# Kernel optimization log

Measured on AMD Instinct MI355X. Metric: run time of the kernel, lower is better.

The kernel has to match this reference:

```python
import jax, jax.numpy as jnp
import numpy as np


def _bilinear_align_corners(img, H, W):
    """Bilinear resize of img [B,K,h,w] to [B,K,H,W], align_corners=True."""
    h, w = img.shape[-2], img.shape[-1]
    ys = jnp.linspace(0.0, h - 1.0, H)
    xs = jnp.linspace(0.0, w - 1.0, W)
    y0 = jnp.clip(jnp.floor(ys).astype(jnp.int32), 0, h - 1)
    y1 = jnp.minimum(y0 + 1, h - 1)
    x0 = jnp.clip(jnp.floor(xs).astype(jnp.int32), 0, w - 1)
    x1 = jnp.minimum(x0 + 1, w - 1)
    wy = (ys - y0.astype(img.dtype))[:, None]   # [H,1]
    wx = (xs - x0.astype(img.dtype))            # [W]
    r0 = img[:, :, y0, :]                        # [B,K,H,w]
    r1 = img[:, :, y1, :]
    top = r0[..., x0] * (1.0 - wx) + r0[..., x1] * wx   # [B,K,H,W]
    bot = r1[..., x0] * (1.0 - wx) + r1[..., x1] * wx
    return top * (1.0 - wy) + bot * wy


def setup_inputs() -> dict:
    key = jax.random.key(0)
    k1, k2, k3 = jax.random.split(key, 3)
    B, C, h, w = 8, 256, 64, 64
    H, W = 512, 512
    K = 21
    feature_map = jax.random.normal(k1, (B, C, h, w), dtype=jnp.float32)
    x = jax.random.uniform(k2, (B, 3, H, W), dtype=jnp.float32)
    W_cls = jax.random.normal(k3, (K, C), dtype=jnp.float32) * 0.02
    b_cls = jnp.zeros((K,), dtype=jnp.float32)
    return {"feature_map": feature_map, "x": x, "W_cls": W_cls, "b_cls": b_cls}


def reference(feature_map, x, W_cls, b_cls):
    # 1x1 conv == channel contraction
    logits = jnp.einsum('bchw,kc->bkhw', feature_map, W_cls) + b_cls[None, :, None, None]
    seg = jax.nn.softmax(logits, axis=1)                      # [B,K,h,w]
    H, W = x.shape[2], x.shape[3]
    seg = _bilinear_align_corners(seg, H, W)                  # [B,K,H,W]
    xi = jnp.transpose(x, (0, 2, 3, 1))                       # [B,H,W,3]
    # q[b,k,c] = mean over (H,W) of x * seg_k  (the per-class loop, fused)
    q = jnp.einsum('bhwc,bkhw->bkc', xi, seg) / (H * W)       # [B,K,3]
    # attn[b,k,h,w] = sum_c x[b,h,w,c] * q[b,k,c]
    segments_by_color = jnp.einsum('bhwc,bkc->bkhw', xi, q)   # [B,K,H,W]
    return segments_by_color
```

## Files before the change

### kernel.cpp

```cpp
#include <hip/hip_runtime.h>
#include <math.h>

#define NB 8
#define NC 256
#define HS 64
#define WSM 64
#define HL 512
#define WL 512
#define NK 21
#define PS (HS*WSM)
#define PL (HL*WL)

#define WT_ELEMS (NK*NC)
#define WT_BLOCKS ((WT_ELEMS+63)/64)

typedef float fx4 __attribute__((ext_vector_type(4)));


__global__ __launch_bounds__(64) void k_prep(
    const float* __restrict__ Wc, float* __restrict__ Wt, float* __restrict__ q)
{
    int blk = blockIdx.x;
    int tid = threadIdx.x;
    if (blk < WT_BLOCKS) {
        int i = blk * 64 + tid;
        if (i < WT_ELEMS) {
            int c = i / NK;
            int k = i - c*NK;
            Wt[c*32 + k] = Wc[k*NC + c];
        }
    } else {
        for (int i = tid; i < NB*NK*3; i += 64) q[i] = 0.f;
    }
}

__global__ __launch_bounds__(256) void k_fused(
    const float* __restrict__ fm, const float* __restrict__ Wt,
    const float* __restrict__ bc, const float* __restrict__ x,
    float* __restrict__ q)
{
    int id = blockIdx.x;
    int swz = (id & 7) * 64 + (id >> 3);
    int b = swz >> 6;
    int h = swz & 63;
    int lane = threadIdx.x & 63;
    int wv   = threadIdx.x >> 6;
    int p = h * 64 + lane;

    __shared__ float tmp[3][WL];
    __shared__ float sA[3][64];
    __shared__ float red[4][NK][64];

    const float scale = 63.0f / 511.0f;
    const float inv_scale = 511.0f / 63.0f;

    if (wv < 3) {
        int Ylo = max(0,    (int)floorf((h - 1) * inv_scale) - 1);
        int Yhi = min(HL-1, (int)ceilf ((h + 1) * inv_scale) + 1);
        const float* xc = x + (size_t)(b*3 + wv) * PL;
        fx4 acc0 = {0.f,0.f,0.f,0.f}, acc1 = {0.f,0.f,0.f,0.f};
        for (int Y = Ylo; Y <= Yhi; ++Y) {
            float fs = Y * scale;
            int i0 = (int)fs; if (i0 > HS-1) i0 = HS-1;
            float f = fs - (float)i0;
            int i1 = min(i0 + 1, HS-1);
            float wt = (i0 == h ? 1.f - f : 0.f) + (i1 == h ? f : 0.f);
            const fx4* xr = (const fx4*)(xc + (size_t)Y * WL);
            acc0 += wt * xr[lane];
            acc1 += wt * xr[lane + 64];
        }
        fx4* t4 = (fx4*)tmp[wv];
        t4[lane]      = acc0;
        t4[lane + 64] = acc1;
        const int w_ = lane;
        int Xlo = max(0,    (int)floorf((w_ - 1) * inv_scale) - 1);
        int Xhi = min(WL-1, (int)ceilf ((w_ + 1) * inv_scale) + 1);
        float a = 0.f;
        for (int X = Xlo; X <= Xhi; ++X) {
            float fs = X * scale;
            int i0 = (int)fs; if (i0 > WSM-1) i0 = WSM-1;
            float f = fs - (float)i0;
            int i1 = min(i0 + 1, WSM-1);
            float wt = (i0 == w_ ? 1.f - f : 0.f) + (i1 == w_ ? f : 0.f);
            a = fmaf(wt, tmp[wv][X], a);
        }
        sA[wv][lane] = a;
    }

    float part[NK];
    #pragma unroll
    for (int k = 0; k < NK; ++k) part[k] = 0.f;

    const float* fmb = fm + (size_t)b * NC * PS + (size_t)(wv * 64) * PS + p;
    #pragma unroll 8
    for (int cc = 0; cc < 64; ++cc) {
        float v = __builtin_nontemporal_load(fmb + (size_t)cc * PS);
        const float* w = Wt + (wv * 64 + cc) * 32;
        #pragma unroll
        for (int k = 0; k < NK; ++k) part[k] = fmaf(v, w[k], part[k]);
    }

    #pragma unroll
    for (int k = 0; k < NK; ++k) red[wv][k][lane] = part[k];
    __syncthreads();

    float logit[NK];
    #pragma unroll
    for (int k = 0; k < NK; ++k)
        logit[k] = bc[k] + ((red[0][k][lane] + red[1][k][lane])
                          + (red[2][k][lane] + red[3][k][lane]));

    float m = logit[0];
    #pragma unroll
    for (int k = 1; k < NK; ++k) m = fmaxf(m, logit[k]);
    float s = 0.f;
    #pragma unroll
    for (int k = 0; k < NK; ++k) { logit[k] = __expf(logit[k] - m); s += logit[k]; }
    float inv = 1.f / s;

    float a0 = sA[0][lane], a1 = sA[1][lane], a2 = sA[2][lane];

    float* qb = q + b * NK * 3;
    for (int k = wv; k < NK; k += 4) {
        float sv = logit[k] * inv;
        float r0 = sv * a0, r1 = sv * a1, r2 = sv * a2;
        #pragma unroll
        for (int off = 32; off; off >>= 1) {
            r0 += __shfl_down(r0, off);
            r1 += __shfl_down(r1, off);
            r2 += __shfl_down(r2, off);
        }
        if (lane == 0) {
            atomicAdd(qb + k*3 + 0, r0);
            atomicAdd(qb + k*3 + 1, r1);
            atomicAdd(qb + k*3 + 2, r2);
        }
    }
}

__global__ __launch_bounds__(256) void k_out(
    const float* __restrict__ x, const float* __restrict__ q,
    float* __restrict__ out)
{
    __shared__ float sq[NK*3];
    int tid = threadIdx.x;
    int b = blockIdx.y;
    if (tid < NK*3) sq[tid] = q[b*NK*3 + tid] * (1.0f / (float)PL);
    __syncthreads();

    int p4 = blockIdx.x * 256 + tid;
    const fx4* xb = (const fx4*)(x + (size_t)b * 3 * PL);
    fx4 x0 = xb[p4];
    fx4 x1 = xb[PL/4 + p4];
    fx4 x2 = xb[2*(PL/4) + p4];
    fx4* ob = (fx4*)(out + (size_t)b * NK * PL);
    #pragma unroll
    for (int k = 0; k < NK; ++k) {
        fx4 o = sq[k*3+0]*x0 + sq[k*3+1]*x1 + sq[k*3+2]*x2;
        __builtin_nontemporal_store(o, ob + (size_t)k * (PL/4) + p4);
    }
}

extern "C" void kernel_launch(void* const* d_in, const int* in_sizes, int n_in,
                              void* d_out, int out_size, void* d_ws, size_t ws_size,
                              hipStream_t stream)
{
    const float* fm = (const float*)d_in[0];
    const float* x  = (const float*)d_in[1];
    const float* Wc = (const float*)d_in[2];
    const float* bc = (const float*)d_in[3];
    float* out = (float*)d_out;

    float* ws = (float*)d_ws;
    float* Wt = ws;
    float* q  = Wt + 8192;

    k_prep<<<WT_BLOCKS + 1, 64, 0, stream>>>(Wc, Wt, q);
    k_fused<<<NB*HS, 256, 0, stream>>>(fm, Wt, bc, x, q);
    k_out<<<dim3(PL/4/256, NB), 256, 0, stream>>>(x, q, out);
}
```

Baseline: 268.8 us.

## Drop prep kernel: stage weights in LDS and replace atomics with partial sums

Removes the separate weight-transpose and zero-init kernel. Each fused block now loads and transposes the classifier weights into shared memory, using a stride of 22, before its channel contraction. Per-row results go to a partials buffer instead of being added atomically. The output kernel then reduces the 64 partials per batch in shared memory before broadcasting q. This saves one launch and the atomic contention, but every block reloads the weights, uses more LDS (which may lower occupancy), and each output block repeats the partial-sum reduction.

```diff
diff --git a/kernel.cpp b/kernel.cpp
--- a/kernel.cpp
+++ b/kernel.cpp
@@ -12,32 +12,14 @@
 #define PL (HL*WL)
 
 #define WT_ELEMS (NK*NC)
-#define WT_BLOCKS ((WT_ELEMS+63)/64)
 
 typedef float fx4 __attribute__((ext_vector_type(4)));
 
 
-__global__ __launch_bounds__(64) void k_prep(
-    const float* __restrict__ Wc, float* __restrict__ Wt, float* __restrict__ q)
-{
-    int blk = blockIdx.x;
-    int tid = threadIdx.x;
-    if (blk < WT_BLOCKS) {
-        int i = blk * 64 + tid;
-        if (i < WT_ELEMS) {
-            int c = i / NK;
-            int k = i - c*NK;
-            Wt[c*32 + k] = Wc[k*NC + c];
-        }
-    } else {
-        for (int i = tid; i < NB*NK*3; i += 64) q[i] = 0.f;
-    }
-}
-
 __global__ __launch_bounds__(256) void k_fused(
-    const float* __restrict__ fm, const float* __restrict__ Wt,
+    const float* __restrict__ fm, const float* __restrict__ Wc,
     const float* __restrict__ bc, const float* __restrict__ x,
-    float* __restrict__ q)
+    float* __restrict__ qpart)
 {
     int id = blockIdx.x;
     int swz = (id & 7) * 64 + (id >> 3);
@@ -47,9 +29,16 @@
     int wv   = threadIdx.x >> 6;
     int p = h * 64 + lane;
 
+    __shared__ float sWt[NC*22];
     __shared__ float tmp[3][WL];
     __shared__ float sA[3][64];
     __shared__ float red[4][NK][64];
+
+    for (int i = threadIdx.x; i < WT_ELEMS; i += 256) {
+        int k = i >> 8;
+        int c = i & 255;
+        sWt[c*22 + k] = Wc[i];
+    }
 
     const float scale = 63.0f / 511.0f;
     const float inv_scale = 511.0f / 63.0f;
@@ -87,6 +76,8 @@
         sA[wv][lane] = a;
     }
 
+    __syncthreads();
+
     float part[NK];
     #pragma unroll
     for (int k = 0; k < NK; ++k) part[k] = 0.f;
@@ -95,7 +86,7 @@
     #pragma unroll 8
     for (int cc = 0; cc < 64; ++cc) {
         float v = __builtin_nontemporal_load(fmb + (size_t)cc * PS);
-        const float* w = Wt + (wv * 64 + cc) * 32;
+        const float* w = sWt + (wv * 64 + cc) * 22;
         #pragma unroll
         for (int k = 0; k < NK; ++k) part[k] = fmaf(v, w[k], part[k]);
     }
@@ -120,7 +111,7 @@
 
     float a0 = sA[0][lane], a1 = sA[1][lane], a2 = sA[2][lane];
 
-    float* qb = q + b * NK * 3;
+    float* qb = qpart + (size_t)(b*64 + h) * 64;
     for (int k = wv; k < NK; k += 4) {
         float sv = logit[k] * inv;
         float r0 = sv * a0, r1 = sv * a1, r2 = sv * a2;
@@ -131,21 +122,32 @@
             r2 += __shfl_down(r2, off);
         }
         if (lane == 0) {
-            atomicAdd(qb + k*3 + 0, r0);
-            atomicAdd(qb + k*3 + 1, r1);
-            atomicAdd(qb + k*3 + 2, r2);
+            qb[k*3 + 0] = r0;
+            qb[k*3 + 1] = r1;
+            qb[k*3 + 2] = r2;
         }
     }
 }
 
 __global__ __launch_bounds__(256) void k_out(
-    const float* __restrict__ x, const float* __restrict__ q,
+    const float* __restrict__ x, const float* __restrict__ qpart,
     float* __restrict__ out)
 {
+    __shared__ float lq[64*64];
     __shared__ float sq[NK*3];
     int tid = threadIdx.x;
     int b = blockIdx.y;
-    if (tid < NK*3) sq[tid] = q[b*NK*3 + tid] * (1.0f / (float)PL);
+
+    const fx4* qp4 = (const fx4*)(qpart + (size_t)b * 64 * 64);
+    fx4* lq4 = (fx4*)lq;
+    #pragma unroll
+    for (int j = 0; j < 4; ++j) lq4[tid + j*256] = qp4[tid + j*256];
+    __syncthreads();
+    if (tid < NK*3) {
+        float s = 0.f;
+        for (int j = 0; j < 64; ++j) s += lq[j*64 + tid];
+        sq[tid] = s * (1.0f / (float)PL);
+    }
     __syncthreads();
 
     int p4 = blockIdx.x * 256 + tid;
@@ -171,11 +173,8 @@
     const float* bc = (const float*)d_in[3];
     float* out = (float*)d_out;
 
-    float* ws = (float*)d_ws;
-    float* Wt = ws;
-    float* q  = Wt + 8192;
+    float* qpart = (float*)d_ws;
 
-    k_prep<<<WT_BLOCKS + 1, 64, 0, stream>>>(Wc, Wt, q);
-    k_fused<<<NB*HS, 256, 0, stream>>>(fm, Wt, bc, x, q);
-    k_out<<<dim3(PL/4/256, NB), 256, 0, stream>>>(x, q, out);
+    k_fused<<<NB*HS, 256, 0, stream>>>(fm, Wc, bc, x, qpart);
+    k_out<<<dim3(PL/4/256, NB), 256, 0, stream>>>(x, qpart, out);
 }
```

New measurement: 237.6 us. 11.6% less time.
